# Performance work log

Measured on AMD Instinct MI355X. Metric: run time of the kernel, lower is better.

## Reference

```python
import jax, jax.numpy as jnp
import numpy as np
from jax import lax

ROI_H = 8        # _ROI_HEIGHT
MAX_BOX = 32     # generator.MAX_BOX
MAX_LEN = 64     # static cap on pooled width/height (replaces dynamic max_width)
SCALE = 8.0      # feature_map_scale
IOU_THR = 0.5    # tf.image.non_max_suppression default
SCORE_THR = 0.3
B, H, W, C = 4, 64, 64, 128


def _reconstruct_boxes(b, scale):
    # b: [B,H,W,4] per-pixel (l,t,r,b) offsets -> absolute (x1,y1,x2,y2) * scale
    Hd, Wd = b.shape[1], b.shape[2]
    xx = jnp.arange(Wd, dtype=b.dtype)[None, None, :]
    yy = jnp.arange(Hd, dtype=b.dtype)[None, :, None]
    left = xx - b[..., 0]
    top = yy - b[..., 1]
    right = xx + b[..., 2]
    bottom = yy + b[..., 3]
    return scale * jnp.stack([left, top, right, bottom], axis=-1)


def _nms_single(bbs, ss):
    # greedy NMS, bbs: [N,4] (x1,y1,x2,y2), ss: [N]; returns [MAX_BOX,4]
    x1, y1, x2, y2 = bbs[:, 0], bbs[:, 1], bbs[:, 2], bbs[:, 3]
    areas = (x2 - x1) * (y2 - y1)

    def body(i, state):
        valid, sel = state
        m = jnp.where(valid, ss, -jnp.inf)
        j = jnp.argmax(m)
        ok = m[j] > -jnp.inf
        sel = sel.at[i].set(jnp.where(ok, j.astype(jnp.int32), -1))
        bj = bbs[j]
        iw = jnp.maximum(jnp.minimum(x2, bj[2]) - jnp.maximum(x1, bj[0]), 0.0)
        ih = jnp.maximum(jnp.minimum(y2, bj[3]) - jnp.maximum(y1, bj[1]), 0.0)
        inter = iw * ih
        iou = inter / (areas + areas[j] - inter + 1e-9)
        valid = valid & (iou <= IOU_THR)   # selected box self-suppresses (iou=1)
        return valid, sel

    N = bbs.shape[0]
    valid0 = jnp.ones((N,), dtype=bool)
    sel0 = jnp.full((MAX_BOX,), -1, dtype=jnp.int32)
    _, sel = lax.fori_loop(0, MAX_BOX, body, (valid0, sel0))
    ok = sel >= 0
    idx = jnp.maximum(sel, 0)
    sb = bbs[idx]
    sc = ss[idx]
    keep = ok & (sc >= SCORE_THR)
    return jnp.where(keep[:, None], sb, jnp.zeros_like(sb))


def _bilinear(img, x, y):
    # img [H,W,C], x [Wp], y [Hp] -> [Hp,Wp,C]; matches TF clip-then-weight behavior
    Hh, Ww = img.shape[0], img.shape[1]
    x0f = jnp.floor(x)
    y0f = jnp.floor(y)
    x0 = jnp.clip(x0f.astype(jnp.int32), 0, Ww - 1)
    x1 = jnp.clip(x0f.astype(jnp.int32) + 1, 0, Ww - 1)
    y0 = jnp.clip(y0f.astype(jnp.int32), 0, Hh - 1)
    y1 = jnp.clip(y0f.astype(jnp.int32) + 1, 0, Hh - 1)
    Ia = img[y0[:, None], x0[None, :]]
    Ib = img[y0[:, None], x1[None, :]]
    Ic = img[y1[:, None], x0[None, :]]
    Id = img[y1[:, None], x1[None, :]]
    x0v, x1v = x0.astype(img.dtype), x1.astype(img.dtype)
    y0v, y1v = y0.astype(img.dtype), y1.astype(img.dtype)
    wa = (x1v - x)[None, :] * (y1v - y)[:, None]
    wb = (x1v - x)[None, :] * (y - y0v)[:, None]
    wc = (x - x0v)[None, :] * (y1v - y)[:, None]
    wd = (x - x0v)[None, :] * (y - y0v)[:, None]
    return (Ia * wa[..., None] + Ib * wb[..., None]
            + Ic * wc[..., None] + Id * wd[..., None])


def _pool_one(img, box, horizontal):
    # img [H,W,C], box [4] in feature-map coords
    w = box[2] - box[0]
    h = box[3] - box[1]
    is_dir = (w >= h) if horizontal else (w < h)
    bz = jnp.where(is_dir, box, jnp.zeros_like(box))
    w = bz[2] - bz[0]
    h = bz[3] - bz[1]
    non_zero = (w >= 0.1) | (h >= 0.1)
    bw = jnp.where(w <= 0.0, 1e-4, w)
    bh = jnp.where(h <= 0.0, 1e-4, h)
    ratio = jnp.where(non_zero, (bw / bh) if horizontal else (bh / bw), 0.0)
    n = jnp.minimum(jnp.ceil(ratio * ROI_H), float(MAX_LEN)).astype(jnp.int32)
    length_f = jnp.maximum(n.astype(img.dtype), 2.0)  # guard div-by-zero for masked boxes
    fmask = non_zero.astype(img.dtype)
    if horizontal:
        map_w = bw / (length_f - 1.0)
        map_h = bh / (ROI_H - 1.0)
        xx = jnp.arange(MAX_LEN, dtype=img.dtype) * map_w + bz[0]
        yy = jnp.arange(ROI_H, dtype=img.dtype) * map_h + bz[1]
        pooled = _bilinear(img, xx, yy)                     # [ROI_H, MAX_LEN, C]
        colmask = (jnp.arange(MAX_LEN) < n).astype(img.dtype) * fmask
        pooled = pooled * colmask[None, :, None]
    else:
        map_w = bw / (ROI_H - 1.0)
        map_h = bh / (length_f - 1.0)
        xx = jnp.arange(ROI_H, dtype=img.dtype) * map_w + bz[0]
        yy = jnp.arange(MAX_LEN, dtype=img.dtype) * map_h + bz[1]
        pooled = _bilinear(img, xx, yy)                     # [MAX_LEN, ROI_H, C]
        rowmask = (jnp.arange(MAX_LEN) < n).astype(img.dtype) * fmask
        pooled = pooled * rowmask[:, None, None]
    return pooled, n


def _roi_pool(fmap, boxes, horizontal):
    # fmap [B,H,W,C], boxes [B,M,4] -> ([B,M,...], [B,M])
    per_img = lambda img, bxs: jax.vmap(lambda b: _pool_one(img, b, horizontal))(bxs)
    return jax.vmap(per_img)(fmap, boxes)


def setup_inputs() -> dict:
    key = jax.random.key(0)
    k1, k2 = jax.random.split(key)
    fmap = jax.random.normal(k1, (B, H, W, C), dtype=jnp.float32)
    # channel 0 -> score logit, channels 1:5 -> positive l/t/r/b offsets in fmap px
    bbox_output = jax.random.uniform(k2, (B, H, W, 5), dtype=jnp.float32) * 3.0
    return {"fmap": fmap, "bbox_output": bbox_output}


def reference(fmap, bbox_output):
    scores = jax.nn.sigmoid(bbox_output[..., 0])                  # [B,H,W]
    boxes = _reconstruct_boxes(bbox_output[..., 1:5], SCALE)      # [B,H,W,4]
    Bn = scores.shape[0]
    bbs = boxes.reshape(Bn, -1, 4)
    ss = scores.reshape(Bn, -1)
    nms_boxes = jax.vmap(_nms_single)(bbs, ss)                    # [B,MAX_BOX,4]
    fb = nms_boxes / SCALE                                        # back to fmap coords
    h_roi, widths = _roi_pool(fmap, fb, True)    # [B,M,8,MAX_LEN,C], [B,M]
    v_roi, heights = _roi_pool(fmap, fb, False)  # [B,M,MAX_LEN,8,C], [B,M]
    return nms_boxes, h_roi, widths, v_roi, heights
```

## Files before the change

### kernel.cpp

```cpp
#include <hip/hip_runtime.h>
#include <hip/hip_bf16.h>
#include <math.h>

#define NPIX 4096
#define MAXB 32
#define NB   4
#define ROI_N 8388608
#define QTOT (ROI_N / 4)

__global__ __launch_bounds__(256) void nms_kernel(const float* __restrict__ bbox,
                                                  float* __restrict__ out_nms,
                                                  float* __restrict__ params,
                                                  float* __restrict__ out_w,
                                                  float* __restrict__ out_hh)
{
    const int b = blockIdx.x;
    const int t = threadIdx.x;

    __shared__ float s_box[NPIX][4];
    __shared__ float s_sel[MAXB][4];
    __shared__ float s_rv[4];
    __shared__ int   s_ri[4];

    float rs[16], rx1[16], ry1[16], rx2[16], ry2[16], rar[16];

    const float* src = bbox + (size_t)b * NPIX * 5;

    #pragma unroll
    for (int i = 0; i < 16; ++i) {
        int p = i * 256 + t;
        int y = p >> 6, x = p & 63;
        float c0 = src[p * 5 + 0];
        float c1 = src[p * 5 + 1];
        float c2 = src[p * 5 + 2];
        float c3 = src[p * 5 + 3];
        float c4 = src[p * 5 + 4];
        float sc = 1.0f / (1.0f + expf(-c0));
        float x1 = 8.0f * ((float)x - c1);
        float y1 = 8.0f * ((float)y - c2);
        float x2 = 8.0f * ((float)x + c3);
        float y2 = 8.0f * ((float)y + c4);
        rs[i] = sc;
        rx1[i] = x1; ry1[i] = y1; rx2[i] = x2; ry2[i] = y2;
        rar[i] = (x2 - x1) * (y2 - y1);
        s_box[p][0] = x1; s_box[p][1] = y1; s_box[p][2] = x2; s_box[p][3] = y2;
    }
    __syncthreads();

    unsigned valid = 0xFFFFu;

    for (int it = 0; it < MAXB; ++it) {
        float best = -INFINITY;
        int   bidx = 0x7FFFFFFF;
        #pragma unroll
        for (int i = 0; i < 16; ++i) {
            float vv  = ((valid >> i) & 1u) ? rs[i] : -INFINITY;
            bool take = vv > best;
            bidx = take ? (i * 256 + t) : bidx;
            best = take ? vv : best;
        }
        #pragma unroll
        for (int off = 32; off; off >>= 1) {
            float ov = __shfl_xor(best, off);
            int   oi = __shfl_xor(bidx, off);
            bool take = (ov > best) || (ov == best && oi < bidx);
            best = take ? ov : best;
            bidx = take ? oi : bidx;
        }
        if ((t & 63) == 0) { s_rv[t >> 6] = best; s_ri[t >> 6] = bidx; }
        __syncthreads();
        best = s_rv[0]; bidx = s_ri[0];
        #pragma unroll
        for (int wv = 1; wv < 4; ++wv) {
            float ov = s_rv[wv]; int oi = s_ri[wv];
            bool take = (ov > best) || (ov == best && oi < bidx);
            best = take ? ov : best;
            bidx = take ? oi : bidx;
        }

        bool ok = (best > -INFINITY);
        int  jj = ok ? bidx : 0;
        float bx1 = s_box[jj][0], by1 = s_box[jj][1];
        float bx2 = s_box[jj][2], by2 = s_box[jj][3];
        float barea = (bx2 - bx1) * (by2 - by1);

        if (t == 0) {
            bool keep = ok && (best >= 0.3f);
            float o0 = keep ? bx1 : 0.f, o1 = keep ? by1 : 0.f;
            float o2 = keep ? bx2 : 0.f, o3 = keep ? by2 : 0.f;
            float* o = out_nms + ((size_t)b * MAXB + it) * 4;
            o[0] = o0; o[1] = o1; o[2] = o2; o[3] = o3;
            s_sel[it][0] = o0; s_sel[it][1] = o1;
            s_sel[it][2] = o2; s_sel[it][3] = o3;
        }

        if (ok) {
            #pragma unroll
            for (int i = 0; i < 16; ++i) {
                float iw = fmaxf(fminf(rx2[i], bx2) - fmaxf(rx1[i], bx1), 0.f);
                float ih = fmaxf(fminf(ry2[i], by2) - fmaxf(ry1[i], by1), 0.f);
                float inter = iw * ih;
                float iou = inter / (rar[i] + barea - inter + 1e-9f);
                valid &= ~(((iou > 0.5f) ? 1u : 0u) << i);
            }
        }
        __syncthreads();
    }

    if (t < 64) {
        int dir = t >> 5, bx = t & 31;
        float x1 = s_sel[bx][0] * 0.125f, y1 = s_sel[bx][1] * 0.125f;
        float x2 = s_sel[bx][2] * 0.125f, y2 = s_sel[bx][3] * 0.125f;
        float w = x2 - x1, h = y2 - y1;
        bool is_dir = (dir == 0) ? (w >= h) : (w < h);
        if (!is_dir) { x1 = 0.f; y1 = 0.f; x2 = 0.f; y2 = 0.f; }
        w = x2 - x1; h = y2 - y1;
        bool  non_zero = (w >= 0.1f) || (h >= 0.1f);
        float bw = (w <= 0.f) ? 1e-4f : w;
        float bh = (h <= 0.f) ? 1e-4f : h;
        float ratio = non_zero ? ((dir == 0) ? __fdiv_rn(bw, bh) : __fdiv_rn(bh, bw)) : 0.f;
        int   n = (int)fminf(ceilf(ratio * 8.0f), 64.0f);
        float length_f = fmaxf((float)n, 2.0f);
        float fmask = non_zero ? 1.f : 0.f;
        float map_w, map_h;
        if (dir == 0) { map_w = __fdiv_rn(bw, length_f - 1.0f); map_h = __fdiv_rn(bh, 7.0f); }
        else          { map_w = __fdiv_rn(bw, 7.0f);            map_h = __fdiv_rn(bh, length_f - 1.0f); }
        int gtb = b * MAXB + bx;
        float* P = params + ((size_t)dir * 128 + gtb) * 8;
        P[0] = x1; P[1] = y1; P[2] = map_w; P[3] = map_h;
        P[4] = (float)n; P[5] = fmask;
        ((dir == 0) ? out_w : out_hh)[gtb] = (float)n;
    }
}

#pragma clang fp contract(off)

__global__ __launch_bounds__(256) void roi_kernel(const float* __restrict__ fmap,
                                                  const float* __restrict__ params,
                                                  float* __restrict__ out_h,
                                                  float* __restrict__ out_v)
{
    int idx = blockIdx.x * 256 + threadIdx.x;
    int dir = (idx >= QTOT) ? 1 : 0;
    int e   = idx - dir * QTOT;
    int tb  = e >> 14;
    int within = e & 16383;
    int pos = within >> 5;
    int ch4 = within & 31;

    const float* P = params + ((size_t)dir * 128 + tb) * 8;
    float bz0x = P[0], bz0y = P[1], map_w = P[2], map_h = P[3];
    int   n     = (int)P[4];
    float fmask = P[5];

    int rr, cc; float mask;
    if (dir == 0) { rr = pos >> 6; cc = pos & 63; mask = (cc < n) ? fmask : 0.f; }
    else          { rr = pos >> 3; cc = pos & 7;  mask = (rr < n) ? fmask : 0.f; }

    int el = (tb << 16) | (pos << 7) | (ch4 << 2);
    float* outp = ((dir == 0) ? out_h : out_v) + el;

    if (mask == 0.f) {
        *(float4*)outp = make_float4(0.f, 0.f, 0.f, 0.f);
        return;
    }

    float x = __fadd_rn(__fmul_rn((float)cc, map_w), bz0x);
    float y = __fadd_rn(__fmul_rn((float)rr, map_h), bz0y);

    float x0f = floorf(x), y0f = floorf(y);
    int ix0 = min(max((int)x0f,     0), 63);
    int ix1 = min(max((int)x0f + 1, 0), 63);
    int iy0 = min(max((int)y0f,     0), 63);
    int iy1 = min(max((int)y0f + 1, 0), 63);

    const float* img = fmap + ((size_t)(tb >> 5)) * (64 * 64 * 128) + (ch4 << 2);
    float4 Ia = *(const float4*)(img + (iy0 * 64 + ix0) * 128);
    float4 Ib = *(const float4*)(img + (iy0 * 64 + ix1) * 128);
    float4 Ic = *(const float4*)(img + (iy1 * 64 + ix0) * 128);
    float4 Id = *(const float4*)(img + (iy1 * 64 + ix1) * 128);

    float x0v = (float)ix0, x1v = (float)ix1;
    float y0v = (float)iy0, y1v = (float)iy1;
    float wa = (x1v - x) * (y1v - y);
    float wb = (x1v - x) * (y - y0v);
    float wc = (x - x0v) * (y1v - y);
    float wd = (x - x0v) * (y - y0v);

    float4 o;
    o.x = (Ia.x * wa + Ib.x * wb + Ic.x * wc + Id.x * wd) * mask;
    o.y = (Ia.y * wa + Ib.y * wb + Ic.y * wc + Id.y * wd) * mask;
    o.z = (Ia.z * wa + Ib.z * wb + Ic.z * wc + Id.z * wd) * mask;
    o.w = (Ia.w * wa + Ib.w * wb + Ic.w * wc + Id.w * wd) * mask;
    *(float4*)outp = o;
}

extern "C" void kernel_launch(void* const* d_in, const int* in_sizes, int n_in,
                              void* d_out, int out_size, void* d_ws, size_t ws_size,
                              hipStream_t stream) {
    const float* fmap = (const float*)d_in[0];
    const float* bbox = (const float*)d_in[1];
    float* out = (float*)d_out;

    float* out_nms = out;
    float* out_h   = out + 512;
    float* out_w   = out_h + ROI_N;
    float* out_v   = out_w + 128;
    float* out_hh  = out_v + ROI_N;

    float* params = (float*)d_ws;

    nms_kernel<<<NB, 256, 0, stream>>>(bbox, out_nms, params, out_w, out_hh);
    roi_kernel<<<(2 * QTOT) / 256, 256, 0, stream>>>(fmap, params, out_h, out_v);
}
```

Before: 145.0 us.

## Fuse NMS suppression into argmax pass and widen ROI threads to eight channels

The NMS loop now applies the previous iteration's IoU suppression inside the same pass that finds the next argmax. It double-buffers the cross-wave reduction slots so one __syncthreads per iteration suffices instead of two. The ROI kernel has each thread handle eight channels with two float4 loads and stores per corner, halving the thread count, and reads the per-box params as two float4 loads. The trade is more register pressure and lower occupancy in the ROI kernel. The NMS path also drops the explicit 'ok' guard and relies on sentinel boxes and clamped indices.

```diff
diff --git a/kernel.cpp b/kernel.cpp
--- a/kernel.cpp
+++ b/kernel.cpp
@@ -1,12 +1,14 @@
 #include <hip/hip_runtime.h>
 #include <hip/hip_bf16.h>
 #include <math.h>
+
+#pragma clang fp contract(off)
 
 #define NPIX 4096
 #define MAXB 32
 #define NB   4
 #define ROI_N 8388608
-#define QTOT (ROI_N / 4)
+#define OTOT (ROI_N / 8)
 
 __global__ __launch_bounds__(256) void nms_kernel(const float* __restrict__ bbox,
                                                   float* __restrict__ out_nms,
@@ -19,8 +21,7 @@
 
     __shared__ float s_box[NPIX][4];
     __shared__ float s_sel[MAXB][4];
-    __shared__ float s_rv[4];
-    __shared__ int   s_ri[4];
+    __shared__ float s_red[2][4][2];
 
     float rs[16], rx1[16], ry1[16], rx2[16], ry2[16], rar[16];
 
@@ -48,13 +49,19 @@
     __syncthreads();
 
     unsigned valid = 0xFFFFu;
+    float wx1 = -1e30f, wy1 = -1e30f, wx2 = -1e30f, wy2 = -1e30f, warea = 0.f;
 
     for (int it = 0; it < MAXB; ++it) {
         float best = -INFINITY;
         int   bidx = 0x7FFFFFFF;
         #pragma unroll
         for (int i = 0; i < 16; ++i) {
-            float vv  = ((valid >> i) & 1u) ? rs[i] : -INFINITY;
+            float iw = fmaxf(fminf(rx2[i], wx2) - fmaxf(rx1[i], wx1), 0.f);
+            float ih = fmaxf(fminf(ry2[i], wy2) - fmaxf(ry1[i], wy1), 0.f);
+            float inter = iw * ih;
+            float iou = __fdiv_rn(inter, rar[i] + warea - inter + 1e-9f);
+            valid &= ~(((iou > 0.5f) ? 1u : 0u) << i);
+            float vv = ((valid >> i) & 1u) ? rs[i] : -INFINITY;
             bool take = vv > best;
             bidx = take ? (i * 256 + t) : bidx;
             best = take ? vv : best;
@@ -67,45 +74,38 @@
             best = take ? ov : best;
             bidx = take ? oi : bidx;
         }
-        if ((t & 63) == 0) { s_rv[t >> 6] = best; s_ri[t >> 6] = bidx; }
+        int buf = it & 1;
+        if ((t & 63) == 0) {
+            s_red[buf][t >> 6][0] = best;
+            s_red[buf][t >> 6][1] = __int_as_float(bidx);
+        }
         __syncthreads();
-        best = s_rv[0]; bidx = s_ri[0];
+        best = s_red[buf][0][0]; bidx = __float_as_int(s_red[buf][0][1]);
         #pragma unroll
         for (int wv = 1; wv < 4; ++wv) {
-            float ov = s_rv[wv]; int oi = s_ri[wv];
+            float ov = s_red[buf][wv][0];
+            int   oi = __float_as_int(s_red[buf][wv][1]);
             bool take = (ov > best) || (ov == best && oi < bidx);
             best = take ? ov : best;
             bidx = take ? oi : bidx;
         }
 
-        bool ok = (best > -INFINITY);
-        int  jj = ok ? bidx : 0;
-        float bx1 = s_box[jj][0], by1 = s_box[jj][1];
-        float bx2 = s_box[jj][2], by2 = s_box[jj][3];
-        float barea = (bx2 - bx1) * (by2 - by1);
+        int jj = min(bidx, NPIX - 1);
+        wx1 = s_box[jj][0]; wy1 = s_box[jj][1];
+        wx2 = s_box[jj][2]; wy2 = s_box[jj][3];
+        warea = (wx2 - wx1) * (wy2 - wy1);
 
         if (t == 0) {
-            bool keep = ok && (best >= 0.3f);
-            float o0 = keep ? bx1 : 0.f, o1 = keep ? by1 : 0.f;
-            float o2 = keep ? bx2 : 0.f, o3 = keep ? by2 : 0.f;
+            bool keep = (best >= 0.3f);
+            float o0 = keep ? wx1 : 0.f, o1 = keep ? wy1 : 0.f;
+            float o2 = keep ? wx2 : 0.f, o3 = keep ? wy2 : 0.f;
             float* o = out_nms + ((size_t)b * MAXB + it) * 4;
             o[0] = o0; o[1] = o1; o[2] = o2; o[3] = o3;
             s_sel[it][0] = o0; s_sel[it][1] = o1;
             s_sel[it][2] = o2; s_sel[it][3] = o3;
         }
-
-        if (ok) {
-            #pragma unroll
-            for (int i = 0; i < 16; ++i) {
-                float iw = fmaxf(fminf(rx2[i], bx2) - fmaxf(rx1[i], bx1), 0.f);
-                float ih = fmaxf(fminf(ry2[i], by2) - fmaxf(ry1[i], by1), 0.f);
-                float inter = iw * ih;
-                float iou = inter / (rar[i] + barea - inter + 1e-9f);
-                valid &= ~(((iou > 0.5f) ? 1u : 0u) << i);
-            }
-        }
-        __syncthreads();
-    }
+    }
+    __syncthreads();
 
     if (t < 64) {
         int dir = t >> 5, bx = t & 31;
@@ -128,12 +128,10 @@
         int gtb = b * MAXB + bx;
         float* P = params + ((size_t)dir * 128 + gtb) * 8;
         P[0] = x1; P[1] = y1; P[2] = map_w; P[3] = map_h;
-        P[4] = (float)n; P[5] = fmask;
+        P[4] = (float)n; P[5] = fmask; P[6] = 0.f; P[7] = 0.f;
         ((dir == 0) ? out_w : out_hh)[gtb] = (float)n;
     }
 }
-
-#pragma clang fp contract(off)
 
 __global__ __launch_bounds__(256) void roi_kernel(const float* __restrict__ fmap,
                                                   const float* __restrict__ params,
@@ -141,27 +139,31 @@
                                                   float* __restrict__ out_v)
 {
     int idx = blockIdx.x * 256 + threadIdx.x;
-    int dir = (idx >= QTOT) ? 1 : 0;
-    int e   = idx - dir * QTOT;
-    int tb  = e >> 14;
-    int within = e & 16383;
-    int pos = within >> 5;
-    int ch4 = within & 31;
-
-    const float* P = params + ((size_t)dir * 128 + tb) * 8;
-    float bz0x = P[0], bz0y = P[1], map_w = P[2], map_h = P[3];
-    int   n     = (int)P[4];
-    float fmask = P[5];
+    int dir = (idx >= OTOT) ? 1 : 0;
+    int e   = idx - dir * OTOT;
+    int tb  = e >> 13;
+    int within = e & 8191;
+    int pos = within >> 4;
+    int ch8 = within & 15;
+
+    const float4* P4 = (const float4*)(params + ((size_t)dir * 128 + tb) * 8);
+    float4 p0 = P4[0];
+    float4 p1 = P4[1];
+    float bz0x = p0.x, bz0y = p0.y, map_w = p0.z, map_h = p0.w;
+    int   n     = (int)p1.x;
+    float fmask = p1.y;
 
     int rr, cc; float mask;
     if (dir == 0) { rr = pos >> 6; cc = pos & 63; mask = (cc < n) ? fmask : 0.f; }
     else          { rr = pos >> 3; cc = pos & 7;  mask = (rr < n) ? fmask : 0.f; }
 
-    int el = (tb << 16) | (pos << 7) | (ch4 << 2);
+    int el = (tb << 16) | (pos << 7) | (ch8 << 3);
     float* outp = ((dir == 0) ? out_h : out_v) + el;
 
     if (mask == 0.f) {
-        *(float4*)outp = make_float4(0.f, 0.f, 0.f, 0.f);
+        float4 z = make_float4(0.f, 0.f, 0.f, 0.f);
+        *(float4*)outp = z;
+        *(float4*)(outp + 4) = z;
         return;
     }
 
@@ -174,11 +176,15 @@
     int iy0 = min(max((int)y0f,     0), 63);
     int iy1 = min(max((int)y0f + 1, 0), 63);
 
-    const float* img = fmap + ((size_t)(tb >> 5)) * (64 * 64 * 128) + (ch4 << 2);
-    float4 Ia = *(const float4*)(img + (iy0 * 64 + ix0) * 128);
-    float4 Ib = *(const float4*)(img + (iy0 * 64 + ix1) * 128);
-    float4 Ic = *(const float4*)(img + (iy1 * 64 + ix0) * 128);
-    float4 Id = *(const float4*)(img + (iy1 * 64 + ix1) * 128);
+    const float* img = fmap + ((size_t)(tb >> 5)) * (64 * 64 * 128) + (ch8 << 3);
+    const float* pa = img + (iy0 * 64 + ix0) * 128;
+    const float* pb = img + (iy0 * 64 + ix1) * 128;
+    const float* pc = img + (iy1 * 64 + ix0) * 128;
+    const float* pd = img + (iy1 * 64 + ix1) * 128;
+    float4 Ia0 = *(const float4*)pa,       Ia1 = *(const float4*)(pa + 4);
+    float4 Ib0 = *(const float4*)pb,       Ib1 = *(const float4*)(pb + 4);
+    float4 Ic0 = *(const float4*)pc,       Ic1 = *(const float4*)(pc + 4);
+    float4 Id0 = *(const float4*)pd,       Id1 = *(const float4*)(pd + 4);
 
     float x0v = (float)ix0, x1v = (float)ix1;
     float y0v = (float)iy0, y1v = (float)iy1;
@@ -187,12 +193,17 @@
     float wc = (x - x0v) * (y1v - y);
     float wd = (x - x0v) * (y - y0v);
 
-    float4 o;
-    o.x = (Ia.x * wa + Ib.x * wb + Ic.x * wc + Id.x * wd) * mask;
-    o.y = (Ia.y * wa + Ib.y * wb + Ic.y * wc + Id.y * wd) * mask;
-    o.z = (Ia.z * wa + Ib.z * wb + Ic.z * wc + Id.z * wd) * mask;
-    o.w = (Ia.w * wa + Ib.w * wb + Ic.w * wc + Id.w * wd) * mask;
-    *(float4*)outp = o;
+    float4 o0, o1;
+    o0.x = (Ia0.x * wa + Ib0.x * wb + Ic0.x * wc + Id0.x * wd) * mask;
+    o0.y = (Ia0.y * wa + Ib0.y * wb + Ic0.y * wc + Id0.y * wd) * mask;
+    o0.z = (Ia0.z * wa + Ib0.z * wb + Ic0.z * wc + Id0.z * wd) * mask;
+    o0.w = (Ia0.w * wa + Ib0.w * wb + Ic0.w * wc + Id0.w * wd) * mask;
+    o1.x = (Ia1.x * wa + Ib1.x * wb + Ic1.x * wc + Id1.x * wd) * mask;
+    o1.y = (Ia1.y * wa + Ib1.y * wb + Ic1.y * wc + Id1.y * wd) * mask;
+    o1.z = (Ia1.z * wa + Ib1.z * wb + Ic1.z * wc + Id1.z * wd) * mask;
+    o1.w = (Ia1.w * wa + Ib1.w * wb + Ic1.w * wc + Id1.w * wd) * mask;
+    *(float4*)outp = o0;
+    *(float4*)(outp + 4) = o1;
 }
 
 extern "C" void kernel_launch(void* const* d_in, const int* in_sizes, int n_in,
@@ -211,5 +222,5 @@
     float* params = (float*)d_ws;
 
     nms_kernel<<<NB, 256, 0, stream>>>(bbox, out_nms, params, out_w, out_hh);
-    roi_kernel<<<(2 * QTOT) / 256, 256, 0, stream>>>(fmap, params, out_h, out_v);
+    roi_kernel<<<(2 * OTOT) / 256, 256, 0, stream>>>(fmap, params, out_h, out_v);
 }
```

After: 139.6 us. -3.8%, faster.
